# Kernel tuning notes

Measured on AMD Instinct MI355X. Metric: run time of the kernel, lower is better.

The kernel has to match this reference:

```python
import jax, jax.numpy as jnp
import numpy as np

B, L, D_MODEL, HEADS, EXP, DEPTH = 2, 2048, 1024, 16, 2, 12
D_EXP = D_MODEL * EXP
D_HEAD = D_EXP // HEADS


def _layernorm(x, g, b, eps=1e-5):
    mu = jnp.mean(x, axis=-1, keepdims=True)
    var = jnp.mean(jnp.square(x - mu), axis=-1, keepdims=True)
    return (x - mu) * jax.lax.rsqrt(var + eps) * g + b


def setup_inputs() -> dict:
    key = jax.random.key(0)
    ks = jax.random.split(key, 4)
    x = jax.random.normal(ks[0], (B, L, D_MODEL), dtype=jnp.float32)
    w_in = jax.random.normal(ks[1], (D_MODEL, 4 * D_EXP), dtype=jnp.float32) * 0.02
    w_out = jax.random.normal(ks[2], (D_EXP, D_MODEL), dtype=jnp.float32) * (0.02 / np.sqrt(2 * DEPTH))
    return {
        "x": x,
        "ln1_g": jnp.ones((D_MODEL,), jnp.float32),
        "ln1_b": jnp.zeros((D_MODEL,), jnp.float32),
        "ln2_g": jnp.ones((D_MODEL,), jnp.float32),
        "ln2_b": jnp.zeros((D_MODEL,), jnp.float32),
        "w_in": w_in,
        "w_out": w_out,
        "smear_factor": jnp.linspace(-6.0, 6.0, HEADS, dtype=jnp.float32),
        "log_scale": jnp.zeros((HEADS,), jnp.float32),
    }


def reference(x, ln1_g, ln1_b, ln2_g, ln2_b, w_in, w_out, smear_factor, log_scale):
    b, l, d = x.shape
    h = smear_factor.shape[0]
    d_exp = w_in.shape[1] // 4
    dh = d_exp // h

    qkvp = _layernorm(x, ln1_g, ln1_b) @ w_in  # [b, l, 4*d_exp]
    q, k, v, p = jnp.split(qkvp, 4, axis=-1)
    # 'b i (h d) -> b h i d'
    to_heads = lambda t: t.reshape(b, l, h, dh).transpose(0, 2, 1, 3)
    q, k, v = to_heads(q), to_heads(k), to_heads(v)

    # smeared keys: k_i <- (1-s)*k_i + s*k_{i-1}  (zero at i=0)
    smear = jax.nn.sigmoid(smear_factor)[None, :, None, None]
    k_prev = jnp.pad(k, ((0, 0), (0, 0), (1, 0), (0, 0)))[:, :, :-1, :]
    k = (1.0 - smear) * k + smear * k_prev

    # ALiBi-style additive mask: slope[h]*j on causal part, -1e10 above diag
    half = h // 2
    slopes = jnp.concatenate([2.0 ** jnp.linspace(0.0, -8.0, half), jnp.zeros((h - half,), jnp.float32)])
    j = jnp.arange(l)
    causal = jnp.where(j[None, :] > j[:, None], jnp.float32(-1e10), jnp.float32(0.0))  # [l, l]
    mask = slopes[:, None, None] * j[None, None, :].astype(jnp.float32) + causal[None, :, :]  # [h, l, l]

    # SDPA with q/s, k/s and default scale 1/sqrt(dh): logits = q k^T / (s^2 sqrt(dh))
    inv = 1.0 / (jnp.exp(2.0 * log_scale)[None, :, None, None] * jnp.sqrt(jnp.float32(dh)))
    logits = jnp.einsum('bhid,bhjd->bhij', q, k) * inv + mask[None]
    attn = jax.nn.softmax(logits, axis=-1)
    o = jnp.einsum('bhij,bhjd->bhid', attn, v)
    o = o.transpose(0, 2, 1, 3).reshape(b, l, h * dh)  # 'b h i d -> b i (h d)'

    out = (jax.nn.silu(p) * o) @ w_out
    return _layernorm(out, ln2_g, ln2_b)
```

## Files before the change

kernel.cpp:

```cpp
#include <hip/hip_runtime.h>

typedef unsigned short u16;
typedef __attribute__((ext_vector_type(8))) short bf16x8;
typedef __attribute__((ext_vector_type(8))) unsigned short u16x8;
typedef __attribute__((ext_vector_type(4))) float f32x4;

#define L_SEQ 2048
#define NTOK 4096
#define DMODEL 1024
#define DEXP 2048
#define NH 16
#define DH 128

__device__ __forceinline__ u16 f2bf(float f) {
    unsigned u = __float_as_uint(f);
    unsigned r = (u + 0x7FFFu + ((u >> 16) & 1u)) >> 16;
    return (u16)r;
}
__device__ __forceinline__ float bf2f(u16 h) {
    return __uint_as_float(((unsigned)h) << 16);
}

template <int CTRL>
__device__ __forceinline__ float dpp_f(float x) {
    return __int_as_float(__builtin_amdgcn_update_dpp(0, __float_as_int(x), CTRL, 0xF, 0xF, true));
}
__device__ __forceinline__ float red16_max(float x) {
    x = fmaxf(x, dpp_f<0xB1>(x));
    x = fmaxf(x, dpp_f<0x4E>(x));
    x = fmaxf(x, dpp_f<0x124>(x));
    x = fmaxf(x, dpp_f<0x128>(x));
    return x;
}

__device__ __forceinline__ void gl_lds16(const u16* g, u16* l) {
    __builtin_amdgcn_global_load_lds((const __attribute__((address_space(1))) void*)g,
                                     (__attribute__((address_space(3))) void*)l, 16, 0, 0);
}

__global__ void conv_transpose(const float* __restrict__ in, u16* __restrict__ out, int R, int C) {
    __shared__ unsigned tile[32][33];
    int c0 = blockIdx.x * 32, r0 = blockIdx.y * 32;
    int tx = threadIdx.x, ty = threadIdx.y;
    for (int j = 0; j < 32; j += 8)
        tile[ty + j][tx] = (unsigned)f2bf(in[(size_t)(r0 + ty + j) * C + c0 + tx]);
    __syncthreads();
    for (int j = 0; j < 32; j += 8)
        out[(size_t)(c0 + ty + j) * R + r0 + tx] = (u16)tile[tx][ty + j];
}

__global__ __launch_bounds__(256) void ln_fwd(const float* __restrict__ x, const float* __restrict__ g,
                                              const float* __restrict__ bta, void* __restrict__ outp,
                                              int out_bf16) {
    int row = blockIdx.x;
    int t = threadIdx.x;
    const float* xr = x + (size_t)row * DMODEL;
    float4 xv = *(const float4*)&xr[t * 4];
    float s = xv.x + xv.y + xv.z + xv.w;
    float s2 = xv.x * xv.x + xv.y * xv.y + xv.z * xv.z + xv.w * xv.w;
    for (int off = 32; off >= 1; off >>= 1) {
        s += __shfl_xor(s, off);
        s2 += __shfl_xor(s2, off);
    }
    __shared__ float red[10];
    int w = t >> 6;
    if ((t & 63) == 0) { red[w] = s; red[4 + w] = s2; }
    __syncthreads();
    if (t == 0) {
        red[8] = red[0] + red[1] + red[2] + red[3];
        red[9] = red[4] + red[5] + red[6] + red[7];
    }
    __syncthreads();
    float mu = red[8] * (1.0f / DMODEL);
    float var = red[9] * (1.0f / DMODEL) - mu * mu;
    float rstd = rsqrtf(var + 1e-5f);
    float vals[4] = {xv.x, xv.y, xv.z, xv.w};
    for (int e = 0; e < 4; e++) {
        int c = t * 4 + e;
        float y = (vals[e] - mu) * rstd * g[c] + bta[c];
        if (out_bf16) ((u16*)outp)[(size_t)row * DMODEL + c] = f2bf(y);
        else          ((float*)outp)[(size_t)row * DMODEL + c] = y;
    }
}

__device__ __forceinline__ void store_out(u16* C, size_t idx, float v) { C[idx] = f2bf(v); }
__device__ __forceinline__ void store_out(float* C, size_t idx, float v) { C[idx] = v; }

template <typename OutT>
__global__ __launch_bounds__(256) void gemm_bt(const u16* __restrict__ A, const u16* __restrict__ BT,
                                               OutT* __restrict__ C, int M, int N, int K) {
    __shared__ u16 a_s[4096];
    __shared__ u16 b_s[4096];
    int tid = threadIdx.x;
    int m0 = blockIdx.y * 128, n0 = blockIdx.x * 128;
    int w = tid >> 6, lane = tid & 63, quad = lane >> 4, ln = lane & 15;
    int wr = (w >> 1) * 64, wc = (w & 1) * 64;
    f32x4 zero4 = {0.f, 0.f, 0.f, 0.f};
    f32x4 acc[4][4];
    for (int r = 0; r < 4; r++)
        for (int c = 0; c < 4; c++) acc[r][c] = zero4;

    int lrow = lane >> 2, lseg = (lane & 3) * 8;
    const u16* Ag0 = A + (size_t)(m0 + 32 * w + lrow) * K + lseg;
    const u16* Ag1 = Ag0 + (size_t)16 * K;
    const u16* Bg0 = BT + (size_t)(n0 + 32 * w + lrow) * K + lseg;
    const u16* Bg1 = Bg0 + (size_t)16 * K;
    u16* al0 = &a_s[(2 * w) * 512];
    u16* al1 = &a_s[(2 * w + 1) * 512];
    u16* bl0 = &b_s[(2 * w) * 512];
    u16* bl1 = &b_s[(2 * w + 1) * 512];

    for (int k0 = 0; k0 < K; k0 += 32) {
        __syncthreads();
        gl_lds16(Ag0 + k0, al0);
        gl_lds16(Ag1 + k0, al1);
        gl_lds16(Bg0 + k0, bl0);
        gl_lds16(Bg1 + k0, bl1);
        __syncthreads();
        bf16x8 af[4], bfr[4];
        for (int r = 0; r < 4; r++) af[r]  = *(const bf16x8*)&a_s[(wr + r * 16 + ln) * 32 + quad * 8];
        for (int c = 0; c < 4; c++) bfr[c] = *(const bf16x8*)&b_s[(wc + c * 16 + ln) * 32 + quad * 8];
        for (int r = 0; r < 4; r++)
            for (int c = 0; c < 4; c++)
                acc[r][c] = __builtin_amdgcn_mfma_f32_16x16x32_bf16(af[r], bfr[c], acc[r][c], 0, 0, 0);
    }
    for (int r = 0; r < 4; r++)
        for (int c = 0; c < 4; c++)
            for (int e = 0; e < 4; e++) {
                int row = m0 + wr + r * 16 + quad * 4 + e;
                int col = n0 + wc + c * 16 + ln;
                store_out(C, (size_t)row * N + col, acc[r][c][e]);
            }
}

__global__ __launch_bounds__(256) void smear_kernel(const u16* __restrict__ qkvp,
                                                    const float* __restrict__ smear_f,
                                                    u16* __restrict__ k_sm) {
    int gid = blockIdx.x * 256 + threadIdx.x;
    int base = gid * 8;
    int bl = base >> 11;
    int c = base & 2047;
    int h = c >> 7;
    int d = c & 127;
    int l = bl & (L_SEQ - 1);
    int bb = bl >> 11;
    float s = 1.0f / (1.0f + __expf(-smear_f[h]));
    u16x8 cur = *(const u16x8*)&qkvp[(size_t)bl * 8192 + 2048 + c];
    u16x8 prv = {0, 0, 0, 0, 0, 0, 0, 0};
    if (l > 0) prv = *(const u16x8*)&qkvp[(size_t)(bl - 1) * 8192 + 2048 + c];
    u16x8 outv;
    for (int u = 0; u < 8; u++) {
        float kc = bf2f(cur[u]);
        float kp = bf2f(prv[u]);
        outv[u] = f2bf((1.0f - s) * kc + s * kp);
    }
    *(u16x8*)&k_sm[(((size_t)(bb * 16 + h)) * L_SEQ + l) * DH + d] = outv;
}

__global__ void vT_kernel(const u16* __restrict__ qkvp, u16* __restrict__ v_t) {
    __shared__ unsigned tile[32][33];
    int l0 = blockIdx.x * 32, d0 = blockIdx.y * 32;
    int bh = blockIdx.z;
    int bb = bh >> 4, h = bh & 15;
    int tx = threadIdx.x, ty = threadIdx.y;
    size_t tokb = (size_t)bb * L_SEQ;
    for (int j = 0; j < 32; j += 8)
        tile[ty + j][tx] = (unsigned)qkvp[(tokb + l0 + ty + j) * 8192 + 4096 + h * DH + d0 + tx];
    __syncthreads();
    for (int j = 0; j < 32; j += 8)
        v_t[((size_t)bh * DH + d0 + ty + j) * L_SEQ + l0 + tx] = (u16)tile[tx][ty + j];
}

__global__ __launch_bounds__(256) void attn_kernel(const u16* __restrict__ qkvp,
                                                   const u16* __restrict__ k_sm,
                                                   const u16* __restrict__ v_t,
                                                   u16* __restrict__ ag2,
                                                   const float* __restrict__ log_scale) {
    __shared__ u16 k_s[16384];
    __shared__ u16 vt_s[16384];
    __shared__ u16 p_s[4608];
    int tid = threadIdx.x;
    int bh = blockIdx.y;
    int bb = bh >> 4, h = bh & 15;
    int w = tid >> 6, lane = tid & 63, quad = lane >> 4, ln = lane & 15;
    size_t tokb = (size_t)bb * L_SEQ;

    const float LOG2E = 1.44269504f;
    float inv = 1.0f / (__expf(2.0f * log_scale[h]) * sqrtf((float)DH));
    float scl = inv * LOG2E;
    float slope2 = ((h < 8) ? exp2f(-8.0f * (float)h / 7.0f) : 0.0f) * LOG2E;

    int lrow = lane >> 2, lcol = lane & 3;
    int lsw8 = (lcol ^ ((lrow >> 1) & 3)) * 8;
    int qsw = (quad ^ ((ln >> 1) & 3)) * 8;
    f32x4 zero4 = {0.f, 0.f, 0.f, 0.f};
    u16* pw = &p_s[w * 1152];
    const short ONE_BF = (short)0x3F80;
    bf16x8 ones = {ONE_BF, ONE_BF, ONE_BF, ONE_BF, ONE_BF, ONE_BF, ONE_BF, ONE_BF};

    for (int sidx = 0; sidx < 2; sidx++) {
        int ib = sidx == 0 ? (31 - (int)blockIdx.x) : (int)blockIdx.x;
        int i0 = ib * 64;
        int si = i0 + w * 16;

        bf16x8 qf[4];
        for (int kt = 0; kt < 4; kt++)
            qf[kt] = *(const bf16x8*)&qkvp[(tokb + si + ln) * 8192 + h * DH + kt * 32 + quad * 8];

        float m_i[4];
        for (int r = 0; r < 4; r++) m_i[r] = -1e30f;
        f32x4 o_acc[8], l_acc;
        for (int dt = 0; dt < 8; dt++) o_acc[dt] = zero4;
        l_acc = zero4;

        const u16* kg[4];
        for (int g = 0; g < 4; g++)
            kg[g] = k_sm + ((size_t)bh * L_SEQ + g * 16 + lrow) * DH + w * 32 + lsw8;
        const u16* vg[4];
        int vloff[4];
        for (int q = 0; q < 4; q++) {
            int c = w * 4 + q;
            int jt = c >> 3, dg = c & 7;
            vg[q] = v_t + ((size_t)bh * DH + dg * 16 + lrow) * L_SEQ + jt * 32 + lsw8;
            vloff[q] = jt * 4096 + dg * 512;
        }

        for (int g = 0; g < 4; g++) { gl_lds16(kg[g], &k_s[w * 2048 + g * 512]); kg[g] += 64 * DH; }
        for (int q = 0; q < 4; q++) { gl_lds16(vg[q], &vt_s[vloff[q]]); vg[q] += 64; }
        __syncthreads();

        int cur = 0;
        for (int j0 = 0; j0 <= i0; j0 += 64) {
            if (j0 + 64 <= i0) {
                int nb = (cur ^ 1) * 8192;
                for (int g = 0; g < 4; g++) { gl_lds16(kg[g], &k_s[nb + w * 2048 + g * 512]); kg[g] += 64 * DH; }
                for (int q = 0; q < 4; q++) { gl_lds16(vg[q], &vt_s[nb + vloff[q]]); vg[q] += 64; }
            }
            const u16* kb = &k_s[cur * 8192];
            const u16* vb = &vt_s[cur * 8192];

            f32x4 sc[4];
            for (int ct = 0; ct < 4; ct++) sc[ct] = zero4;
            __builtin_amdgcn_s_setprio(1);
            for (int kt = 0; kt < 4; kt++)
                for (int ct = 0; ct < 4; ct++) {
                    bf16x8 bfr = *(const bf16x8*)&kb[kt * 2048 + (ct * 16 + ln) * 32 + qsw];
                    sc[ct] = __builtin_amdgcn_mfma_f32_16x16x32_bf16(qf[kt], bfr, sc[ct], 0, 0, 0);
                }
            __builtin_amdgcn_s_setprio(0);

            bool full = (j0 + 63 <= si);
            float s2[4][4];
            float aj0 = slope2 * (float)(j0 + ln);
            for (int ct = 0; ct < 4; ct++) {
                float ajv = aj0 + slope2 * (float)(16 * ct);
                int j = j0 + ct * 16 + ln;
                for (int r = 0; r < 4; r++) {
                    float v = fmaf(sc[ct][r], scl, ajv);
                    if (!full) {
                        int i = si + quad * 4 + r;
                        if (j > i) v = -3.0e38f;
                    }
                    s2[ct][r] = v;
                }
            }
            float alpha[4];
            bool any_resc = false;
            for (int r = 0; r < 4; r++) {
                float mr = fmaxf(fmaxf(s2[0][r], s2[1][r]), fmaxf(s2[2][r], s2[3][r]));
                mr = red16_max(mr);
                float mnew = fmaxf(m_i[r], mr);
                alpha[r] = exp2f(m_i[r] - mnew);
                any_resc |= (alpha[r] != 1.0f);
                m_i[r] = mnew;
                for (int ct = 0; ct < 4; ct++) {
                    float p = exp2f(s2[ct][r] - mnew);
                    u16 pb = (u16)(__float_as_uint(p) >> 16);
                    pw[(quad * 4 + r) * 72 + ct * 16 + ln] = pb;
                }
            }
            if (__any(any_resc)) {
                for (int dt = 0; dt < 8; dt++) {
                    f32x4 o = o_acc[dt];
                    for (int r = 0; r < 4; r++) o[r] *= alpha[r];
                    o_acc[dt] = o;
                }
                for (int r = 0; r < 4; r++) l_acc[r] *= alpha[r];
            }
            asm volatile("s_waitcnt lgkmcnt(0)" ::: "memory");
            __builtin_amdgcn_s_setprio(1);
            for (int ks = 0; ks < 2; ks++) {
                bf16x8 pa = *(const bf16x8*)&pw[ln * 72 + ks * 32 + quad * 8];
                l_acc = __builtin_amdgcn_mfma_f32_16x16x32_bf16(pa, ones, l_acc, 0, 0, 0);
                for (int dt = 0; dt < 8; dt++) {
                    bf16x8 vf = *(const bf16x8*)&vb[ks * 4096 + (dt * 16 + ln) * 32 + qsw];
                    o_acc[dt] = __builtin_amdgcn_mfma_f32_16x16x32_bf16(pa, vf, o_acc[dt], 0, 0, 0);
                }
            }
            __builtin_amdgcn_s_setprio(0);
            __syncthreads();
            cur ^= 1;
        }

        float rinv[4];
        for (int r = 0; r < 4; r++) rinv[r] = __builtin_amdgcn_rcpf(l_acc[r]);
        for (int dt = 0; dt < 8; dt++)
            for (int r = 0; r < 4; r++) {
                int i = si + quad * 4 + r;
                int dcol = dt * 16 + ln;
                float o = o_acc[dt][r] * rinv[r];
                float pv = bf2f(qkvp[(tokb + i) * 8192 + 6144 + h * DH + dcol]);
                float gate = pv * __builtin_amdgcn_rcpf(1.0f + exp2f(-pv * LOG2E));
                ag2[(tokb + i) * 2048 + h * DH + dcol] = f2bf(gate * o);
            }
    }
}

extern "C" void kernel_launch(void* const* d_in, const int* in_sizes, int n_in,
                              void* d_out, int out_size, void* d_ws, size_t ws_size,
                              hipStream_t stream) {
    const float* x       = (const float*)d_in[0];
    const float* ln1_g   = (const float*)d_in[1];
    const float* ln1_b   = (const float*)d_in[2];
    const float* ln2_g   = (const float*)d_in[3];
    const float* ln2_b   = (const float*)d_in[4];
    const float* w_in    = (const float*)d_in[5];
    const float* w_out   = (const float*)d_in[6];
    const float* smear_f = (const float*)d_in[7];
    const float* logsc   = (const float*)d_in[8];
    float* out = (float*)d_out;
    char* ws = (char*)d_ws;

    u16* w_inT   = (u16*)(ws + 0);
    u16* w_outT  = (u16*)(ws + (size_t)16777216);
    u16* lnA     = (u16*)(ws + (size_t)20971520);
    u16* qkvp    = (u16*)(ws + (size_t)29360128);
    u16* k_sm    = (u16*)(ws + (size_t)96468992);
    u16* ag2     = (u16*)(ws + (size_t)113246208);
    float* out_pre = (float*)(ws + (size_t)96468992);
    u16* v_t     = (u16*)(ws + 0);

    dim3 b32x8(32, 8);
    conv_transpose<<<dim3(8192 / 32, 1024 / 32), b32x8, 0, stream>>>(w_in, w_inT, 1024, 8192);
    conv_transpose<<<dim3(1024 / 32, 2048 / 32), b32x8, 0, stream>>>(w_out, w_outT, 2048, 1024);
    ln_fwd<<<NTOK, 256, 0, stream>>>(x, ln1_g, ln1_b, (void*)lnA, 1);
    gemm_bt<u16><<<dim3(8192 / 128, 4096 / 128), 256, 0, stream>>>(lnA, w_inT, qkvp, NTOK, 8192, 1024);
    smear_kernel<<<4096, 256, 0, stream>>>(qkvp, smear_f, k_sm);
    vT_kernel<<<dim3(L_SEQ / 32, DH / 32, 32), b32x8, 0, stream>>>(qkvp, v_t);
    attn_kernel<<<dim3(16, 32), 256, 0, stream>>>(qkvp, k_sm, v_t, ag2, logsc);
    gemm_bt<float><<<dim3(1024 / 128, 4096 / 128), 256, 0, stream>>>(ag2, w_outT, out_pre, NTOK, 1024, 2048);
    ln_fwd<<<NTOK, 256, 0, stream>>>(out_pre, ln2_g, ln2_b, (void*)out, 0);
}
```

Before: 395.1 us.

## Single-strip attention blocks with smaller LDS, higher occupancy, XCD-aware mapping

Each attention block now handles one 64-row query strip instead of a paired long and short strip, so the grid doubles to 1024 blocks. K/V tiles become single-buffered, which halves LDS use, and launch bounds request 4 blocks per CU so that occupancy, not explicit double buffering, hides load latency. Block indices are remapped so each XCD processes a fixed set of heads, for L2 locality, and strips are ordered longest first. The P scratch buffer switches from padded rows to an XOR-swizzled layout. The cost is losing the prefetch overlap and the paired-strip load balancing, with extra barriers per tile.

```diff
diff --git a/kernel.cpp b/kernel.cpp
--- a/kernel.cpp
+++ b/kernel.cpp
@@ -171,16 +171,19 @@
         v_t[((size_t)bh * DH + d0 + ty + j) * L_SEQ + l0 + tx] = (u16)tile[tx][ty + j];
 }
 
-__global__ __launch_bounds__(256) void attn_kernel(const u16* __restrict__ qkvp,
-                                                   const u16* __restrict__ k_sm,
-                                                   const u16* __restrict__ v_t,
-                                                   u16* __restrict__ ag2,
-                                                   const float* __restrict__ log_scale) {
-    __shared__ u16 k_s[16384];
-    __shared__ u16 vt_s[16384];
-    __shared__ u16 p_s[4608];
+__global__ __launch_bounds__(256, 4) void attn_kernel(const u16* __restrict__ qkvp,
+                                                      const u16* __restrict__ k_sm,
+                                                      const u16* __restrict__ v_t,
+                                                      u16* __restrict__ ag2,
+                                                      const float* __restrict__ log_scale) {
+    __shared__ u16 k_s[8192];
+    __shared__ u16 vt_s[8192];
+    __shared__ u16 p_s[4096];
     int tid = threadIdx.x;
-    int bh = blockIdx.y;
+    int xcd = blockIdx.x & 7, slot = blockIdx.x >> 3;
+    int bh = xcd * 4 + ((int)blockIdx.y & 3);
+    int strip = slot * 8 + ((int)blockIdx.y >> 2);
+    int ib = 31 - strip;
     int bb = bh >> 4, h = bh & 15;
     int w = tid >> 6, lane = tid & 63, quad = lane >> 4, ln = lane & 15;
     size_t tokb = (size_t)bb * L_SEQ;
@@ -194,126 +197,116 @@
     int lsw8 = (lcol ^ ((lrow >> 1) & 3)) * 8;
     int qsw = (quad ^ ((ln >> 1) & 3)) * 8;
     f32x4 zero4 = {0.f, 0.f, 0.f, 0.f};
-    u16* pw = &p_s[w * 1152];
+    u16* pw = &p_s[w * 1024];
     const short ONE_BF = (short)0x3F80;
     bf16x8 ones = {ONE_BF, ONE_BF, ONE_BF, ONE_BF, ONE_BF, ONE_BF, ONE_BF, ONE_BF};
 
-    for (int sidx = 0; sidx < 2; sidx++) {
-        int ib = sidx == 0 ? (31 - (int)blockIdx.x) : (int)blockIdx.x;
-        int i0 = ib * 64;
-        int si = i0 + w * 16;
-
-        bf16x8 qf[4];
-        for (int kt = 0; kt < 4; kt++)
-            qf[kt] = *(const bf16x8*)&qkvp[(tokb + si + ln) * 8192 + h * DH + kt * 32 + quad * 8];
-
-        float m_i[4];
-        for (int r = 0; r < 4; r++) m_i[r] = -1e30f;
-        f32x4 o_acc[8], l_acc;
-        for (int dt = 0; dt < 8; dt++) o_acc[dt] = zero4;
-        l_acc = zero4;
-
-        const u16* kg[4];
-        for (int g = 0; g < 4; g++)
-            kg[g] = k_sm + ((size_t)bh * L_SEQ + g * 16 + lrow) * DH + w * 32 + lsw8;
-        const u16* vg[4];
-        int vloff[4];
-        for (int q = 0; q < 4; q++) {
-            int c = w * 4 + q;
-            int jt = c >> 3, dg = c & 7;
-            vg[q] = v_t + ((size_t)bh * DH + dg * 16 + lrow) * L_SEQ + jt * 32 + lsw8;
-            vloff[q] = jt * 4096 + dg * 512;
-        }
-
+    int i0 = ib * 64;
+    int si = i0 + w * 16;
+
+    bf16x8 qf[4];
+    for (int kt = 0; kt < 4; kt++)
+        qf[kt] = *(const bf16x8*)&qkvp[(tokb + si + ln) * 8192 + h * DH + kt * 32 + quad * 8];
+
+    float m_i[4];
+    for (int r = 0; r < 4; r++) m_i[r] = -1e30f;
+    f32x4 o_acc[8], l_acc;
+    for (int dt = 0; dt < 8; dt++) o_acc[dt] = zero4;
+    l_acc = zero4;
+
+    const u16* kg[4];
+    for (int g = 0; g < 4; g++)
+        kg[g] = k_sm + ((size_t)bh * L_SEQ + g * 16 + lrow) * DH + w * 32 + lsw8;
+    const u16* vg[4];
+    int vloff[4];
+    for (int q = 0; q < 4; q++) {
+        int c = w * 4 + q;
+        int jt = c >> 3, dg = c & 7;
+        vg[q] = v_t + ((size_t)bh * DH + dg * 16 + lrow) * L_SEQ + jt * 32 + lsw8;
+        vloff[q] = jt * 4096 + dg * 512;
+    }
+
+    for (int j0 = 0; j0 <= i0; j0 += 64) {
+        __syncthreads();
         for (int g = 0; g < 4; g++) { gl_lds16(kg[g], &k_s[w * 2048 + g * 512]); kg[g] += 64 * DH; }
         for (int q = 0; q < 4; q++) { gl_lds16(vg[q], &vt_s[vloff[q]]); vg[q] += 64; }
         __syncthreads();
 
-        int cur = 0;
-        for (int j0 = 0; j0 <= i0; j0 += 64) {
-            if (j0 + 64 <= i0) {
-                int nb = (cur ^ 1) * 8192;
-                for (int g = 0; g < 4; g++) { gl_lds16(kg[g], &k_s[nb + w * 2048 + g * 512]); kg[g] += 64 * DH; }
-                for (int q = 0; q < 4; q++) { gl_lds16(vg[q], &vt_s[nb + vloff[q]]); vg[q] += 64; }
-            }
-            const u16* kb = &k_s[cur * 8192];
-            const u16* vb = &vt_s[cur * 8192];
-
-            f32x4 sc[4];
-            for (int ct = 0; ct < 4; ct++) sc[ct] = zero4;
-            __builtin_amdgcn_s_setprio(1);
-            for (int kt = 0; kt < 4; kt++)
-                for (int ct = 0; ct < 4; ct++) {
-                    bf16x8 bfr = *(const bf16x8*)&kb[kt * 2048 + (ct * 16 + ln) * 32 + qsw];
-                    sc[ct] = __builtin_amdgcn_mfma_f32_16x16x32_bf16(qf[kt], bfr, sc[ct], 0, 0, 0);
+        f32x4 sc[4];
+        for (int ct = 0; ct < 4; ct++) sc[ct] = zero4;
+        __builtin_amdgcn_s_setprio(1);
+        for (int kt = 0; kt < 4; kt++)
+            for (int ct = 0; ct < 4; ct++) {
+                bf16x8 bfr = *(const bf16x8*)&k_s[kt * 2048 + (ct * 16 + ln) * 32 + qsw];
+                sc[ct] = __builtin_amdgcn_mfma_f32_16x16x32_bf16(qf[kt], bfr, sc[ct], 0, 0, 0);
+            }
+        __builtin_amdgcn_s_setprio(0);
+
+        bool full = (j0 + 63 <= si);
+        float s2[4][4];
+        float aj0 = slope2 * (float)(j0 + ln);
+        for (int ct = 0; ct < 4; ct++) {
+            float ajv = aj0 + slope2 * (float)(16 * ct);
+            int j = j0 + ct * 16 + ln;
+            for (int r = 0; r < 4; r++) {
+                float v = fmaf(sc[ct][r], scl, ajv);
+                if (!full) {
+                    int i = si + quad * 4 + r;
+                    if (j > i) v = -3.0e38f;
                 }
-            __builtin_amdgcn_s_setprio(0);
-
-            bool full = (j0 + 63 <= si);
-            float s2[4][4];
-            float aj0 = slope2 * (float)(j0 + ln);
+                s2[ct][r] = v;
+            }
+        }
+        float alpha[4];
+        bool any_resc = false;
+        for (int r = 0; r < 4; r++) {
+            float mr = fmaxf(fmaxf(s2[0][r], s2[1][r]), fmaxf(s2[2][r], s2[3][r]));
+            mr = red16_max(mr);
+            float mnew = fmaxf(m_i[r], mr);
+            alpha[r] = exp2f(m_i[r] - mnew);
+            any_resc |= (alpha[r] != 1.0f);
+            m_i[r] = mnew;
+            int row = quad * 4 + r;
+            int rk = row & 7;
             for (int ct = 0; ct < 4; ct++) {
-                float ajv = aj0 + slope2 * (float)(16 * ct);
-                int j = j0 + ct * 16 + ln;
-                for (int r = 0; r < 4; r++) {
-                    float v = fmaf(sc[ct][r], scl, ajv);
-                    if (!full) {
-                        int i = si + quad * 4 + r;
-                        if (j > i) v = -3.0e38f;
-                    }
-                    s2[ct][r] = v;
-                }
-            }
-            float alpha[4];
-            bool any_resc = false;
-            for (int r = 0; r < 4; r++) {
-                float mr = fmaxf(fmaxf(s2[0][r], s2[1][r]), fmaxf(s2[2][r], s2[3][r]));
-                mr = red16_max(mr);
-                float mnew = fmaxf(m_i[r], mr);
-                alpha[r] = exp2f(m_i[r] - mnew);
-                any_resc |= (alpha[r] != 1.0f);
-                m_i[r] = mnew;
-                for (int ct = 0; ct < 4; ct++) {
-                    float p = exp2f(s2[ct][r] - mnew);
-                    u16 pb = (u16)(__float_as_uint(p) >> 16);
-                    pw[(quad * 4 + r) * 72 + ct * 16 + ln] = pb;
-                }
-            }
-            if (__any(any_resc)) {
-                for (int dt = 0; dt < 8; dt++) {
-                    f32x4 o = o_acc[dt];
-                    for (int r = 0; r < 4; r++) o[r] *= alpha[r];
-                    o_acc[dt] = o;
-                }
-                for (int r = 0; r < 4; r++) l_acc[r] *= alpha[r];
-            }
-            asm volatile("s_waitcnt lgkmcnt(0)" ::: "memory");
-            __builtin_amdgcn_s_setprio(1);
-            for (int ks = 0; ks < 2; ks++) {
-                bf16x8 pa = *(const bf16x8*)&pw[ln * 72 + ks * 32 + quad * 8];
-                l_acc = __builtin_amdgcn_mfma_f32_16x16x32_bf16(pa, ones, l_acc, 0, 0, 0);
-                for (int dt = 0; dt < 8; dt++) {
-                    bf16x8 vf = *(const bf16x8*)&vb[ks * 4096 + (dt * 16 + ln) * 32 + qsw];
-                    o_acc[dt] = __builtin_amdgcn_mfma_f32_16x16x32_bf16(pa, vf, o_acc[dt], 0, 0, 0);
-                }
-            }
-            __builtin_amdgcn_s_setprio(0);
-            __syncthreads();
-            cur ^= 1;
-        }
-
-        float rinv[4];
-        for (int r = 0; r < 4; r++) rinv[r] = __builtin_amdgcn_rcpf(l_acc[r]);
-        for (int dt = 0; dt < 8; dt++)
-            for (int r = 0; r < 4; r++) {
-                int i = si + quad * 4 + r;
-                int dcol = dt * 16 + ln;
-                float o = o_acc[dt][r] * rinv[r];
-                float pv = bf2f(qkvp[(tokb + i) * 8192 + 6144 + h * DH + dcol]);
-                float gate = pv * __builtin_amdgcn_rcpf(1.0f + exp2f(-pv * LOG2E));
-                ag2[(tokb + i) * 2048 + h * DH + dcol] = f2bf(gate * o);
-            }
-    }
+                float p = exp2f(s2[ct][r] - mnew);
+                u16 pb = (u16)(__float_as_uint(p) >> 16);
+                int sl = ct * 2 + (ln >> 3);
+                pw[row * 64 + ((sl ^ rk) << 3) + (ln & 7)] = pb;
+            }
+        }
+        if (__any(any_resc)) {
+            for (int dt = 0; dt < 8; dt++) {
+                f32x4 o = o_acc[dt];
+                for (int r = 0; r < 4; r++) o[r] *= alpha[r];
+                o_acc[dt] = o;
+            }
+            for (int r = 0; r < 4; r++) l_acc[r] *= alpha[r];
+        }
+        asm volatile("s_waitcnt lgkmcnt(0)" ::: "memory");
+        __builtin_amdgcn_s_setprio(1);
+        for (int ks = 0; ks < 2; ks++) {
+            bf16x8 pa = *(const bf16x8*)&pw[ln * 64 + (((ks * 4 + quad) ^ (ln & 7)) << 3)];
+            l_acc = __builtin_amdgcn_mfma_f32_16x16x32_bf16(pa, ones, l_acc, 0, 0, 0);
+            for (int dt = 0; dt < 8; dt++) {
+                bf16x8 vf = *(const bf16x8*)&vt_s[ks * 4096 + (dt * 16 + ln) * 32 + qsw];
+                o_acc[dt] = __builtin_amdgcn_mfma_f32_16x16x32_bf16(pa, vf, o_acc[dt], 0, 0, 0);
+            }
+        }
+        __builtin_amdgcn_s_setprio(0);
+    }
+
+    float rinv[4];
+    for (int r = 0; r < 4; r++) rinv[r] = __builtin_amdgcn_rcpf(l_acc[r]);
+    for (int dt = 0; dt < 8; dt++)
+        for (int r = 0; r < 4; r++) {
+            int i = si + quad * 4 + r;
+            int dcol = dt * 16 + ln;
+            float o = o_acc[dt][r] * rinv[r];
+            float pv = bf2f(qkvp[(tokb + i) * 8192 + 6144 + h * DH + dcol]);
+            float gate = pv * __builtin_amdgcn_rcpf(1.0f + exp2f(-pv * LOG2E));
+            ag2[(tokb + i) * 2048 + h * DH + dcol] = f2bf(gate * o);
+        }
 }
 
 extern "C" void kernel_launch(void* const* d_in, const int* in_sizes, int n_in,
@@ -347,7 +340,7 @@
     gemm_bt<u16><<<dim3(8192 / 128, 4096 / 128), 256, 0, stream>>>(lnA, w_inT, qkvp, NTOK, 8192, 1024);
     smear_kernel<<<4096, 256, 0, stream>>>(qkvp, smear_f, k_sm);
     vT_kernel<<<dim3(L_SEQ / 32, DH / 32, 32), b32x8, 0, stream>>>(qkvp, v_t);
-    attn_kernel<<<dim3(16, 32), 256, 0, stream>>>(qkvp, k_sm, v_t, ag2, logsc);
+    attn_kernel<<<dim3(32, 32), 256, 0, stream>>>(qkvp, k_sm, v_t, ag2, logsc);
     gemm_bt<float><<<dim3(1024 / 128, 4096 / 128), 256, 0, stream>>>(ag2, w_outT, out_pre, NTOK, 1024, 2048);
     ln_fwd<<<NTOK, 256, 0, stream>>>(out_pre, ln2_g, ln2_b, (void*)out, 0);
 }
```

Result: no change. 392.5 us (-0.7%).

## Remap GEMM and attention blocks across XCDs and use lazy softmax rescaling

Applied to the files above, without the earlier changes.

Remaps block indices in the GEMM and attention kernels so that blocks sharing the same N-columns or the same head land on the same XCD, which improves L2 reuse of weights and K/V. The online softmax now rescales the accumulators only when the running max grows by more than 8 in log2 units, rather than on every increase, so it skips the per-tile alpha computation and the O/l multiplies in most iterations. The lazy rescale lets p values exceed 1 (up to 2^8) in bf16, which trades a little precision for fewer rescales. The XCD mapping assumes the grid x-dimension is divisible by 8 and that the attention grid has the expected shape.

```diff
diff --git a/kernel.cpp b/kernel.cpp
--- a/kernel.cpp
+++ b/kernel.cpp
@@ -92,7 +92,13 @@
     __shared__ u16 a_s[4096];
     __shared__ u16 b_s[4096];
     int tid = threadIdx.x;
-    int m0 = blockIdx.y * 128, n0 = blockIdx.x * 128;
+    unsigned NX = gridDim.x;
+    unsigned lin = blockIdx.x + NX * blockIdx.y;
+    unsigned per = NX >> 3;
+    unsigned xcd = lin & 7, t = lin >> 3;
+    unsigned n_p = xcd * per + (t % per);
+    unsigned m_p = t / per;
+    int m0 = m_p * 128, n0 = n_p * 128;
     int w = tid >> 6, lane = tid & 63, quad = lane >> 4, ln = lane & 15;
     int wr = (w >> 1) * 64, wc = (w & 1) * 64;
     f32x4 zero4 = {0.f, 0.f, 0.f, 0.f};
@@ -180,7 +186,10 @@
     __shared__ u16 vt_s[16384];
     __shared__ u16 p_s[4608];
     int tid = threadIdx.x;
-    int bh = blockIdx.y;
+    unsigned lin = blockIdx.x + 16u * blockIdx.y;
+    unsigned xcd = lin & 7, tt = lin >> 3;
+    int bh = (int)(xcd * 4 + (tt & 3));
+    int pair = (int)(tt >> 2);
     int bb = bh >> 4, h = bh & 15;
     int w = tid >> 6, lane = tid & 63, quad = lane >> 4, ln = lane & 15;
     size_t tokb = (size_t)bb * L_SEQ;
@@ -199,7 +208,7 @@
     bf16x8 ones = {ONE_BF, ONE_BF, ONE_BF, ONE_BF, ONE_BF, ONE_BF, ONE_BF, ONE_BF};
 
     for (int sidx = 0; sidx < 2; sidx++) {
-        int ib = sidx == 0 ? (31 - (int)blockIdx.x) : (int)blockIdx.x;
+        int ib = sidx == 0 ? (31 - pair) : pair;
         int i0 = ib * 64;
         int si = i0 + w * 16;
 
@@ -264,28 +273,34 @@
                     s2[ct][r] = v;
                 }
             }
-            float alpha[4];
-            bool any_resc = false;
+            float pm[4];
+            bool need = false;
             for (int r = 0; r < 4; r++) {
                 float mr = fmaxf(fmaxf(s2[0][r], s2[1][r]), fmaxf(s2[2][r], s2[3][r]));
                 mr = red16_max(mr);
-                float mnew = fmaxf(m_i[r], mr);
-                alpha[r] = exp2f(m_i[r] - mnew);
-                any_resc |= (alpha[r] != 1.0f);
-                m_i[r] = mnew;
-                for (int ct = 0; ct < 4; ct++) {
-                    float p = exp2f(s2[ct][r] - mnew);
-                    u16 pb = (u16)(__float_as_uint(p) >> 16);
-                    pw[(quad * 4 + r) * 72 + ct * 16 + ln] = pb;
-                }
-            }
-            if (__any(any_resc)) {
+                pm[r] = mr;
+                need |= (mr - m_i[r] > 8.0f);
+            }
+            if (__any(need)) {
+                float alpha[4];
+                for (int r = 0; r < 4; r++) {
+                    float mnew = fmaxf(m_i[r], pm[r]);
+                    alpha[r] = exp2f(m_i[r] - mnew);
+                    m_i[r] = mnew;
+                }
                 for (int dt = 0; dt < 8; dt++) {
                     f32x4 o = o_acc[dt];
                     for (int r = 0; r < 4; r++) o[r] *= alpha[r];
                     o_acc[dt] = o;
                 }
                 for (int r = 0; r < 4; r++) l_acc[r] *= alpha[r];
+            }
+            for (int r = 0; r < 4; r++) {
+                for (int ct = 0; ct < 4; ct++) {
+                    float p = exp2f(s2[ct][r] - m_i[r]);
+                    u16 pb = (u16)(__float_as_uint(p) >> 16);
+                    pw[(quad * 4 + r) * 72 + ct * 16 + ln] = pb;
+                }
             }
             asm volatile("s_waitcnt lgkmcnt(0)" ::: "memory");
             __builtin_amdgcn_s_setprio(1);
```

Result: faster. 379.3 us (-4.0%).
